# Performance work log

Hardware: AMD Instinct MI355X
Metric: run time of the kernel (lower is better)

The kernel has to match this reference:

```python
import jax, jax.numpy as jnp
import numpy as np

# Model hyperparams (match init_kwargs)
B, T, CIN, COUT = 4, 12, 4, 4
P = 16; HIMG = WIMG = 256; HP = WP = 16
D = 384; L = 4; DFF = 4 * D; MAXG = 0.3
CPLX = jnp.complex64

# NOTE: RiemannianCliffordConv2d / TemporalPropagator / FluxTracker / basis /
# encoder / decoder sources were not provided; they are reconstructed here as
# faithful-structure surrogates: plain conv2d for the Clifford conv, complex
# linear eigen-basis encode/decode, exp-decay scan operators, complex FFN,
# patch-embed conv encoder and per-patch linear decoder. sde_mode='ode' so the
# stochastic branch is skipped, matching the explicit guard in the source.

def _ln(x, g, b):
    m = x.mean(-1, keepdims=True)
    v = jnp.var(x, axis=-1, keepdims=True)
    return (x - m) * jax.lax.rsqrt(v + 1e-5) * g + b

def _conv(x, w, b, stride, pad):
    y = jax.lax.conv_general_dilated(x, w, (stride, stride), pad,
                                     dimension_numbers=('NCHW', 'OIHW', 'NCHW'))
    return y + b[None, :, None, None]

def _pscan(A, X):
    # first-order linear recurrence h_t = A_t*h_{t-1} + X_t via associative scan over axis=1
    def comb(l, r):
        al, xl = l; ar, xr = r
        return al * ar, xl * ar + xr
    return jax.lax.associative_scan(comb, (A, X), axis=1)[1]

def _cgelu(z):
    return jax.nn.gelu(z.real) + 1j * jax.nn.gelu(z.imag)

def _model(x, dt, enc_w, enc_b, ns_g, ns_b, cw, cb, nt_g, nt_b,
           E_re, E_im, Ei_re, Ei_im, lam_flux, Ws_re, Ws_im, Wg, nu, omega,
           w1_re, w1_im, w2_re, w2_im, dec_w, dec_b):
    Bx, Tx = x.shape[0], x.shape[1]
    # ---- encoder: patch-embed conv -> complex latent (B,T,D,HP,WP)
    xf = x.reshape(Bx * Tx, CIN, HIMG, WIMG)
    e = _conv(xf, enc_w, enc_b, P, 'VALID')              # (BT, 2D, HP, WP)
    zr, zi = jnp.split(e, 2, axis=1)
    z = (zr + 1j * zi).astype(CPLX).reshape(Bx, Tx, D, HP, WP)
    for i in range(L):
        E = E_re[i] + 1j * E_im[i]
        Ei = Ei_re[i] + 1j * Ei_im[i]
        Ws = Ws_re[i] + 1j * Ws_im[i]
        W1 = w1_re[i] + 1j * w1_im[i]
        W2 = w2_re[i] + 1j * w2_im[i]
        # ---- _apply_spatial (residual Clifford conv on stacked re/im)
        xflat = z.reshape(Bx * Tx, D, HP, WP)
        xr2 = jnp.concatenate([xflat.real, xflat.imag], axis=1)   # (BT,2D,H,W)
        xn = jnp.transpose(xr2, (0, 2, 3, 1))
        xn = _ln(xn, ns_g[i], ns_b[i])
        xn = jnp.transpose(xn, (0, 3, 1, 2))
        xs = _conv(xn, cw[i], cb[i], 1, 'SAME')
        sre, sim = jnp.split(xs, 2, axis=1)
        xflat = xflat + (sre + 1j * sim)
        z = xflat.reshape(Bx, Tx, D, HP, WP)
        # ---- eigen-basis encode
        xp = jnp.transpose(z, (0, 1, 3, 4, 2))                    # (B,T,H,W,D)
        x_eig = jnp.einsum('bthwd,de->bthwe', xp, E)
        x_mean = x_eig.mean(axis=(2, 3))                          # (B,T,D)
        # ---- flux tracker scan (states start at zero => flux_prev term vanishes)
        a = jnp.exp(-jax.nn.softplus(lam_flux[i])[None, None] * dt[..., None])
        A_flux = a.astype(CPLX)
        X_flux = x_mean * dt[..., None]
        flux = _pscan(A_flux, X_flux)                             # (B,T,D) complex
        source = jnp.einsum('btd,de->bte', flux, Ws)
        gate = jax.nn.sigmoid(flux.real * Wg[i][None, None])      # (B,T,D) real
        g = gate[:, :, None, None, :]
        forcing = x_eig * g + source[:, :, None, None, :] * (1.0 - g)
        # ---- transition operators and temporal pscan
        lam = jnp.clip(-jax.nn.softplus(nu[i]), -5.0, MAXG) + 1j * omega[i]  # (D,)
        op_decay = jnp.exp(lam[None, None] * dt[..., None])       # (B,T,D) complex
        op_forcing = (op_decay - 1.0) / lam
        u_t = forcing * op_forcing[:, :, None, None, :]           # (B,T,H,W,D)
        # h_prev is zero-initialized per _init_states => its t0 contribution is zero
        A_full = jnp.broadcast_to(op_decay[:, :, None, None, :], u_t.shape)
        u_out = _pscan(A_full, u_t)                               # (B,T,H,W,D)
        # ---- decode + temporal FFN residual
        decoded = jnp.einsum('bthwd,de->bthwe', u_out, Ei)
        dec5 = jnp.transpose(decoded, (0, 1, 4, 2, 3))            # (B,T,D,H,W)
        df = dec5.reshape(Bx * Tx, D, HP, WP)
        dr = jnp.concatenate([df.real, df.imag], axis=1)
        dn = _ln(jnp.transpose(dr, (0, 2, 3, 1)), nt_g[i], nt_b[i])
        dn = jnp.transpose(dn, (0, 3, 1, 2))
        nre, nim = jnp.split(dn, 2, axis=1)
        xcl = jnp.transpose(nre + 1j * nim, (0, 2, 3, 1))          # (BT,H,W,D)
        delta = jnp.einsum('bhwf,fd->bhwd', _cgelu(jnp.einsum('bhwd,df->bhwf', xcl, W1)), W2)
        delta = jnp.transpose(delta, (0, 3, 1, 2))
        x_out = (df + delta).reshape(Bx, Tx, D, HP, WP)
        z = z + x_out
    # ---- ensemble decoder (mean member): per-patch linear head + depth-to-space
    feats = jnp.concatenate([z.real, z.imag], axis=2)             # (B,T,2D,H,W)
    fl = jnp.transpose(feats, (0, 1, 3, 4, 2))                    # (B,T,H,W,2D)
    y = jnp.einsum('bthwc,oc->bthwo', fl, dec_w) + dec_b
    y = y.reshape(Bx, Tx, HP, WP, COUT, P, P)
    y = jnp.transpose(y, (0, 1, 4, 2, 5, 3, 6)).reshape(Bx, Tx, COUT, HP * P, WP * P)
    return y


def setup_inputs() -> dict:
    key = jax.random.key(0)
    ks = jax.random.split(key, 32)
    s = 0.02
    d = {}
    d['x'] = jax.random.normal(ks[0], (B, T, CIN, HIMG, WIMG), dtype=jnp.float32)
    d['dt'] = jax.random.uniform(ks[1], (B, T), minval=0.5, maxval=1.5, dtype=jnp.float32)
    d['enc_w'] = jax.random.normal(ks[2], (2 * D, CIN, P, P), dtype=jnp.float32) * s
    d['enc_b'] = jnp.zeros((2 * D,), jnp.float32)
    d['ns_g'] = jnp.ones((L, 2 * D), jnp.float32)
    d['ns_b'] = jnp.zeros((L, 2 * D), jnp.float32)
    d['cw'] = jax.random.normal(ks[3], (L, 2 * D, 2 * D, 3, 3), dtype=jnp.float32) * s
    d['cb'] = jnp.zeros((L, 2 * D), jnp.float32)
    d['nt_g'] = jnp.ones((L, 2 * D), jnp.float32)
    d['nt_b'] = jnp.zeros((L, 2 * D), jnp.float32)
    d['E_re'] = jax.random.normal(ks[4], (L, D, D), dtype=jnp.float32) * s
    d['E_im'] = jax.random.normal(ks[5], (L, D, D), dtype=jnp.float32) * s
    d['Ei_re'] = jax.random.normal(ks[6], (L, D, D), dtype=jnp.float32) * s
    d['Ei_im'] = jax.random.normal(ks[7], (L, D, D), dtype=jnp.float32) * s
    d['lam_flux'] = jax.random.normal(ks[8], (L, D), dtype=jnp.float32)
    d['Ws_re'] = jax.random.normal(ks[9], (L, D, D), dtype=jnp.float32) * s
    d['Ws_im'] = jax.random.normal(ks[10], (L, D, D), dtype=jnp.float32) * s
    d['Wg'] = jax.random.normal(ks[11], (L, D), dtype=jnp.float32)
    d['nu'] = jax.random.normal(ks[12], (L, D), dtype=jnp.float32)
    d['omega'] = jax.random.normal(ks[13], (L, D), dtype=jnp.float32) * 0.5
    d['w1_re'] = jax.random.normal(ks[14], (L, D, DFF), dtype=jnp.float32) * s
    d['w1_im'] = jax.random.normal(ks[15], (L, D, DFF), dtype=jnp.float32) * s
    d['w2_re'] = jax.random.normal(ks[16], (L, DFF, D), dtype=jnp.float32) * s
    d['w2_im'] = jax.random.normal(ks[17], (L, DFF, D), dtype=jnp.float32) * s
    d['dec_w'] = jax.random.normal(ks[18], (COUT * P * P, 2 * D), dtype=jnp.float32) * s
    d['dec_b'] = jnp.zeros((COUT * P * P,), jnp.float32)
    return d


def reference(x, dt, enc_w, enc_b, ns_g, ns_b, cw, cb, nt_g, nt_b,
              E_re, E_im, Ei_re, Ei_im, lam_flux, Ws_re, Ws_im, Wg, nu, omega,
              w1_re, w1_im, w2_re, w2_im, dec_w, dec_b):
    return _model(x, dt, enc_w, enc_b, ns_g, ns_b, cw, cb, nt_g, nt_b,
                  E_re, E_im, Ei_re, Ei_im, lam_flux, Ws_re, Ws_im, Wg, nu, omega,
                  w1_re, w1_im, w2_re, w2_im, dec_w, dec_b)
```

## Files before the change

kernel.cpp:

```cpp
#include <hip/hip_runtime.h>
#include <cstddef>
#include <cstdint>

typedef unsigned short u16;
typedef short bf16x8 __attribute__((ext_vector_type(8)));
typedef float f32x4 __attribute__((ext_vector_type(4)));

__device__ __forceinline__ float gelu_tanh(float x) {
  float x3 = x * x * x;
  float t = tanhf(0.7978845608028654f * (x + 0.044715f * x3));
  return 0.5f * x * (1.0f + t);
}
__device__ __forceinline__ float softplus_f(float x) {
  return (x > 20.0f) ? x : log1pf(expf(x));
}
__device__ __forceinline__ u16 f2bf(float f) {
  uint32_t u = __float_as_uint(f);
  uint32_t r = (u + 0x7fffu + ((u >> 16) & 1u)) >> 16;
  return (u16)r;
}

__device__ __forceinline__ void gload16(const u16* g, u16* l) {
  __builtin_amdgcn_global_load_lds(
      (const __attribute__((address_space(1))) void*)g,
      (__attribute__((address_space(3))) void*)l, 16, 0, 0);
}

template <int TN, int MODE>
__global__ __launch_bounds__(256) void gemm_kernel(
    const u16* __restrict__ A, const u16* __restrict__ Bt, int K, int ldc,
    float* __restrict__ Cf, u16* __restrict__ Cb,
    const float* __restrict__ bias, const float* __restrict__ Df) {
  __shared__ u16 As[2][128 * 32];
  __shared__ u16 Bs[2][TN * 32];
  constexpr int NI = (TN == 64) ? 2 : 4;
  const int m0 = blockIdx.x * 128, n0 = blockIdx.y * TN;
  const int tid = threadIdx.x;
  const int lane = tid & 63, w = tid >> 6;
  const int lane15 = lane & 15, quad = lane >> 4;
  const int r0 = lane >> 2, e0 = (lane & 3) * 8;
  const int wy = (TN == 64) ? w : (w >> 1);
  const int wx = (TN == 64) ? 0 : (w & 1);

  const u16* ag0 = A + (size_t)(m0 + w * 32 + r0) * K + e0;
  const u16* ag1 = ag0 + (size_t)16 * K;
  const u16* bg0 = (TN == 64) ? Bt + (size_t)(n0 + w * 16 + r0) * K + e0
                              : Bt + (size_t)(n0 + w * 32 + r0) * K + e0;
  const u16* bg1 = bg0 + (size_t)16 * K;

  f32x4 acc[NI][4] = {};
  const int abase = (wy * (16 * NI) + lane15) * 32 + quad * 8;
  const int bbase = (wx * 64 + lane15) * 32 + quad * 8;

  for (int k0 = 0; k0 < K; k0 += 64) {
#pragma unroll
    for (int p = 0; p < 2; ++p) {
      const int kk = k0 + 32 * p;
      gload16(ag0 + kk, &As[p][w * 1024]);
      gload16(ag1 + kk, &As[p][w * 1024 + 512]);
      if (TN == 64) {
        gload16(bg0 + kk, &Bs[p][w * 512]);
      } else {
        gload16(bg0 + kk, &Bs[p][w * 1024]);
        gload16(bg1 + kk, &Bs[p][w * 1024 + 512]);
      }
    }
    __syncthreads();
#pragma unroll
    for (int p = 0; p < 2; ++p) {
      bf16x8 af[NI], bf[4];
#pragma unroll
      for (int i = 0; i < NI; ++i) af[i] = *(const bf16x8*)&As[p][abase + i * 16 * 32];
#pragma unroll
      for (int j = 0; j < 4; ++j) bf[j] = *(const bf16x8*)&Bs[p][bbase + j * 16 * 32];
#pragma unroll
      for (int i = 0; i < NI; ++i)
#pragma unroll
        for (int j = 0; j < 4; ++j)
          acc[i][j] = __builtin_amdgcn_mfma_f32_16x16x32_bf16(af[i], bf[j], acc[i][j], 0, 0, 0);
    }
    __syncthreads();
  }

  const int mw = m0 + wy * (16 * NI), nw = n0 + wx * 64;
#pragma unroll
  for (int i = 0; i < NI; ++i) {
#pragma unroll
    for (int j = 0; j < 4; ++j) {
      const int col = nw + j * 16 + lane15;
#pragma unroll
      for (int r = 0; r < 4; ++r) {
        const int row = mw + i * 16 + quad * 4 + r;
        const float v = acc[i][j][r];
        const size_t idx = (size_t)row * ldc + col;
        if (MODE == 0) {
          Cf[idx] = v;
        } else if (MODE == 1) {
          Cb[idx] = f2bf(gelu_tanh(v));
        } else if (MODE == 2) {
          Cf[idx] += v;
        } else if (MODE == 3) {
          const int frame = row >> 8, pix = row & 255;
          const int hp = pix >> 4, wp = pix & 15;
          const int co = col >> 8, p1 = (col >> 4) & 15, p2 = col & 15;
          Cf[(((size_t)frame * 4 + co) * 256 + hp * 16 + p1) * 256 + wp * 16 + p2] = v + bias[col];
        } else if (MODE == 4) {
          Cf[idx] += v + Df[idx];
        } else if (MODE == 5) {
          const float nz = Cf[idx] + v;
          Cf[idx] = nz;
          Cb[idx] = f2bf(nz);
        }
      }
    }
  }
}

__global__ __launch_bounds__(256) void conv_mfma_kernel(
    const u16* __restrict__ xnp, const u16* __restrict__ Btc,
    const float* __restrict__ cbias,
    float* __restrict__ z, u16* __restrict__ zb) {
  __shared__ u16 As[2][128 * 32];
  __shared__ u16 Bs[2][128 * 32];
  const int m0 = blockIdx.x * 128, n0 = blockIdx.y * 128;
  const int tid = threadIdx.x;
  const int lane = tid & 63, w = tid >> 6;
  const int lane15 = lane & 15, quad = lane >> 4;
  const int r0 = lane >> 2, e0 = (lane & 3) * 8;

  const int rowA0 = m0 + w * 32 + r0, rowA1 = rowA0 + 16;
  const long long cen0 = ((long long)(rowA0 >> 8) * 324 + ((((rowA0 & 255) >> 4) + 1) * 18) + (rowA0 & 15) + 1) * 768 + e0;
  const long long cen1 = ((long long)(rowA1 >> 8) * 324 + ((((rowA1 & 255) >> 4) + 1) * 18) + (rowA1 & 15) + 1) * 768 + e0;
  const u16* bg0 = Btc + (size_t)(n0 + w * 32 + r0) * 6912 + e0;
  const u16* bg1 = bg0 + (size_t)16 * 6912;

  f32x4 acc[4][4] = {};
  const int wy = w >> 1, wx = w & 1;
  const int abase = (wy * 64 + lane15) * 32 + quad * 8;
  const int bbase = (wx * 64 + lane15) * 32 + quad * 8;

  for (int tap = 0; tap < 9; ++tap) {
    const int doff = ((tap / 3 - 1) * 18 + (tap % 3 - 1)) * 768;
    const u16* a0 = xnp + cen0 + doff;
    const u16* a1 = xnp + cen1 + doff;
    const u16* b0 = bg0 + tap * 768;
    const u16* b1 = bg1 + tap * 768;
    for (int kc = 0; kc < 768; kc += 64) {
#pragma unroll
      for (int p = 0; p < 2; ++p) {
        const int kk = kc + 32 * p;
        gload16(a0 + kk, &As[p][w * 1024]);
        gload16(a1 + kk, &As[p][w * 1024 + 512]);
        gload16(b0 + kk, &Bs[p][w * 1024]);
        gload16(b1 + kk, &Bs[p][w * 1024 + 512]);
      }
      __syncthreads();
#pragma unroll
      for (int p = 0; p < 2; ++p) {
        bf16x8 af[4], bf[4];
#pragma unroll
        for (int i = 0; i < 4; ++i) af[i] = *(const bf16x8*)&As[p][abase + i * 16 * 32];
#pragma unroll
        for (int j = 0; j < 4; ++j) bf[j] = *(const bf16x8*)&Bs[p][bbase + j * 16 * 32];
#pragma unroll
        for (int i = 0; i < 4; ++i)
#pragma unroll
          for (int j = 0; j < 4; ++j)
            acc[i][j] = __builtin_amdgcn_mfma_f32_16x16x32_bf16(af[i], bf[j], acc[i][j], 0, 0, 0);
      }
      __syncthreads();
    }
  }

  const int mw = m0 + wy * 64, nw = n0 + wx * 64;
#pragma unroll
  for (int i = 0; i < 4; ++i) {
#pragma unroll
    for (int j = 0; j < 4; ++j) {
      const int col = nw + j * 16 + lane15;
      const float bv = cbias[col];
#pragma unroll
      for (int r = 0; r < 4; ++r) {
        const int row = mw + i * 16 + quad * 4 + r;
        const size_t idx = (size_t)row * 768 + col;
        const float nz = z[idx] + acc[i][j][r] + bv;
        z[idx] = nz;
        zb[idx] = f2bf(nz);
      }
    }
  }
}

__global__ __launch_bounds__(256) void encoder_mfma_kernel(
    const float* __restrict__ x, const float* __restrict__ ew,
    const float* __restrict__ eb, float* __restrict__ z) {
  __shared__ u16 As[128 * 32];
  __shared__ u16 Bs[128 * 32];
  const int m0 = blockIdx.x * 128, n0 = blockIdx.y * 128;
  const int tid = threadIdx.x;
  const int lane = tid & 63, w = tid >> 6;
  const int lane15 = lane & 15, quad = lane >> 4;
  const int srow = tid >> 1, half = tid & 1;
  const int arow = m0 + srow;
  const int frame = arow >> 8, pix = arow & 255, hh = pix >> 4, ww = pix & 15;

  f32x4 acc[4][4] = {};
  const int wy = w >> 1, wx = w & 1;
  const int ar_base = (wy * 64 + lane15) * 32 + quad * 8;
  const int br_base = (wx * 64 + lane15) * 32 + quad * 8;

  for (int k0 = 0; k0 < 1024; k0 += 32) {
    const int gk = k0 + half * 16;
    const int c = gk >> 8, ph = (gk >> 4) & 15;
    const float* ax = x + (((size_t)(frame * 4 + c) * 256 + hh * 16 + ph) * 256 + ww * 16);
    const float* bx = ew + (size_t)(n0 + srow) * 1024 + gk;
    u16 ta[16], tb[16];
#pragma unroll
    for (int j = 0; j < 4; ++j) {
      const float4 va = *(const float4*)(ax + j * 4);
      const float4 vb = *(const float4*)(bx + j * 4);
      ta[j * 4 + 0] = f2bf(va.x); ta[j * 4 + 1] = f2bf(va.y);
      ta[j * 4 + 2] = f2bf(va.z); ta[j * 4 + 3] = f2bf(va.w);
      tb[j * 4 + 0] = f2bf(vb.x); tb[j * 4 + 1] = f2bf(vb.y);
      tb[j * 4 + 2] = f2bf(vb.z); tb[j * 4 + 3] = f2bf(vb.w);
    }
    __syncthreads();
    *(uint4*)&As[srow * 32 + half * 16] = *(uint4*)ta;
    *(uint4*)&As[srow * 32 + half * 16 + 8] = *(uint4*)(ta + 8);
    *(uint4*)&Bs[srow * 32 + half * 16] = *(uint4*)tb;
    *(uint4*)&Bs[srow * 32 + half * 16 + 8] = *(uint4*)(tb + 8);
    __syncthreads();
    bf16x8 af[4], bfv[4];
#pragma unroll
    for (int i = 0; i < 4; ++i) af[i] = *(const bf16x8*)&As[ar_base + i * 16 * 32];
#pragma unroll
    for (int j = 0; j < 4; ++j) bfv[j] = *(const bf16x8*)&Bs[br_base + j * 16 * 32];
#pragma unroll
    for (int i = 0; i < 4; ++i)
#pragma unroll
      for (int j = 0; j < 4; ++j)
        acc[i][j] = __builtin_amdgcn_mfma_f32_16x16x32_bf16(af[i], bfv[j], acc[i][j], 0, 0, 0);
  }

  const int mw = m0 + wy * 64, nw = n0 + wx * 64;
#pragma unroll
  for (int i = 0; i < 4; ++i)
#pragma unroll
    for (int j = 0; j < 4; ++j) {
      const int col = nw + j * 16 + lane15;
      const float bv = eb[col];
#pragma unroll
      for (int r = 0; r < 4; ++r) {
        const int row = mw + i * 16 + quad * 4 + r;
        z[(size_t)row * 768 + col] = acc[i][j][r] + bv;
      }
    }
}

__global__ __launch_bounds__(256) void expand_kernel(
    const float* __restrict__ Wre, const float* __restrict__ Wim,
    int ldw, int Kc, int Nc, u16* __restrict__ Wt) {
  __shared__ float tile[32][33];
  const int k0 = blockIdx.x * 32, n0 = blockIdx.y * 32;
  const bool khi = k0 >= Kc, nhi = n0 >= Nc;
  const float* src = (khi != nhi) ? Wim : Wre;
  const float sgn = (!nhi && khi) ? -1.0f : 1.0f;
  const int sk = k0 - (khi ? Kc : 0), sn = n0 - (nhi ? Nc : 0);
  const int c = threadIdx.x & 31, r8 = threadIdx.x >> 5;
  for (int r = r8; r < 32; r += 8)
    tile[r][c] = src[(size_t)(sk + r) * ldw + sn + c];
  __syncthreads();
  const int twoK = 2 * Kc;
  for (int r = r8; r < 32; r += 8)
    Wt[(size_t)(n0 + r) * twoK + k0 + c] = f2bf(sgn * tile[c][r]);
}

__global__ __launch_bounds__(256) void reorder_cw_kernel(
    const float* __restrict__ cwl, u16* __restrict__ Btc) {
  __shared__ float buf[6912];
  const int o = blockIdx.x;
  const float* src = cwl + (size_t)o * 6912;
  for (int i = threadIdx.x; i < 6912; i += 256) buf[i] = src[i];
  __syncthreads();
  u16* dst = Btc + (size_t)o * 6912;
  for (int i = threadIdx.x; i < 6912; i += 256) {
    const int tap = i / 768, cc = i - tap * 768;
    dst[i] = f2bf(buf[cc * 9 + tap]);
  }
}

__global__ __launch_bounds__(256) void cast_bf16_kernel(
    const float* __restrict__ in, u16* __restrict__ out, int n) {
  const int g = blockIdx.x * 256 + threadIdx.x;
  if (g < n) out[g] = f2bf(in[g]);
}

template <bool HALO>
__global__ __launch_bounds__(192) void ln_kernel(
    const float* __restrict__ in, const float* __restrict__ g,
    const float* __restrict__ b, u16* __restrict__ out) {
  const int row = blockIdx.x, tid = threadIdx.x;
  const float4 v = *(const float4*)(in + (size_t)row * 768 + tid * 4);
  float s = v.x + v.y + v.z + v.w;
  float q = v.x * v.x + v.y * v.y + v.z * v.z + v.w * v.w;
#pragma unroll
  for (int off = 32; off > 0; off >>= 1) {
    s += __shfl_down(s, off);
    q += __shfl_down(q, off);
  }
  __shared__ float rs[3], rq[3];
  if ((tid & 63) == 0) { rs[tid >> 6] = s; rq[tid >> 6] = q; }
  __syncthreads();
  const float S = rs[0] + rs[1] + rs[2], Q = rq[0] + rq[1] + rq[2];
  const float mean = S * (1.0f / 768.0f);
  const float inv = rsqrtf(Q * (1.0f / 768.0f) - mean * mean + 1e-5f);
  const float4 gv = *(const float4*)(g + tid * 4);
  const float4 bv = *(const float4*)(b + tid * 4);
  u16 p[4];
  p[0] = f2bf((v.x - mean) * inv * gv.x + bv.x);
  p[1] = f2bf((v.y - mean) * inv * gv.y + bv.y);
  p[2] = f2bf((v.z - mean) * inv * gv.z + bv.z);
  p[3] = f2bf((v.w - mean) * inv * gv.w + bv.w);
  size_t base;
  if (HALO) {
    const int f = row >> 8, pp = row & 255, h = pp >> 4, ww = pp & 15;
    base = ((size_t)f * 324 + (h + 1) * 18 + ww + 1) * 768;
  } else {
    base = (size_t)row * 768;
  }
  *(uint2*)(out + base + tid * 4) = *(uint2*)p;
}

__global__ __launch_bounds__(768) void mean_kernel(
    const float* __restrict__ eig, float* __restrict__ mr, float* __restrict__ mi) {
  const int f = blockIdx.x, c = threadIdx.x;
  const float* p = eig + (size_t)f * 256 * 768 + c;
  float s0 = 0.f, s1 = 0.f, s2 = 0.f, s3 = 0.f;
  for (int px = 0; px < 256; px += 4) {
    s0 += p[(size_t)px * 768];
    s1 += p[(size_t)(px + 1) * 768];
    s2 += p[(size_t)(px + 2) * 768];
    s3 += p[(size_t)(px + 3) * 768];
  }
  const float tot = (s0 + s1 + s2 + s3) * (1.0f / 256.0f);
  if (c < 384) mr[f * 384 + c] = tot;
  else         mi[f * 384 + c - 384] = tot;
}

__global__ __launch_bounds__(384) void flux_kernel(
    const float* __restrict__ dt, const float* __restrict__ lamf,
    const float* __restrict__ nu, const float* __restrict__ omega,
    const float* __restrict__ mr, const float* __restrict__ mi,
    float* __restrict__ fluxr, float* __restrict__ fluxi,
    float* __restrict__ opdr, float* __restrict__ opdi,
    float* __restrict__ opfr, float* __restrict__ opfi) {
  const int b = blockIdx.x;
  const int d = threadIdx.x;
  const float sp = softplus_f(lamf[d]);
  float lre = -softplus_f(nu[d]);
  lre = fmaxf(lre, -5.0f);
  const float lim = omega[d];
  const float den = lre * lre + lim * lim;
  float fr = 0.f, fi = 0.f;
  for (int t = 0; t < 12; ++t) {
    const float dtv = dt[b * 12 + t];
    const int idx = (b * 12 + t) * 384 + d;
    const float A = expf(-sp * dtv);
    fr = A * fr + mr[idx] * dtv;
    fi = A * fi + mi[idx] * dtv;
    fluxr[idx] = fr; fluxi[idx] = fi;
    const float ed = expf(lre * dtv);
    const float odr = ed * cosf(lim * dtv);
    const float odi = ed * sinf(lim * dtv);
    opdr[idx] = odr; opdi[idx] = odi;
    const float nr_ = odr - 1.0f, ni_ = odi;
    opfr[idx] = (nr_ * lre + ni_ * lim) / den;
    opfi[idx] = (ni_ * lre - nr_ * lim) / den;
  }
}

#define SBM 64
#define SBN 64
#define SBK 32
__global__ __launch_bounds__(256) void cgemm_src_kernel(
    const float* __restrict__ Ar, const float* __restrict__ Ai, int lda,
    const float* __restrict__ Wr, const float* __restrict__ Wi, int ldw,
    const float* __restrict__ Wg,
    float* __restrict__ G, float* __restrict__ SGr, float* __restrict__ SGi,
    int ldc, int M, int K) {
  __shared__ float Asr[SBK][SBM], Asi[SBK][SBM];
  __shared__ float Wsr[SBK][SBN], Wsi[SBK][SBN];
  const int m0 = blockIdx.x * SBM;
  const int n0 = blockIdx.y * SBN;
  const int tid = threadIdx.x;
  const int tn = tid & 15, tm = tid >> 4;
  float accr[4][4] = {}, acci[4][4] = {};
  for (int k0 = 0; k0 < K; k0 += SBK) {
    for (int s = tid; s < 512; s += 256) {
      {
        int r = s >> 3, kk = (s & 7) << 2;
        int row = m0 + r;
        float4 vr = {0.f, 0.f, 0.f, 0.f}, vi = {0.f, 0.f, 0.f, 0.f};
        if (row < M) {
          vr = *(const float4*)(Ar + (size_t)row * lda + k0 + kk);
          vi = *(const float4*)(Ai + (size_t)row * lda + k0 + kk);
        }
        Asr[kk + 0][r] = vr.x; Asr[kk + 1][r] = vr.y; Asr[kk + 2][r] = vr.z; Asr[kk + 3][r] = vr.w;
        Asi[kk + 0][r] = vi.x; Asi[kk + 1][r] = vi.y; Asi[kk + 2][r] = vi.z; Asi[kk + 3][r] = vi.w;
      }
      {
        int wr_ = s >> 4, wc = (s & 15) << 2;
        *(float4*)&Wsr[wr_][wc] = *(const float4*)(Wr + (size_t)(k0 + wr_) * ldw + n0 + wc);
        *(float4*)&Wsi[wr_][wc] = *(const float4*)(Wi + (size_t)(k0 + wr_) * ldw + n0 + wc);
      }
    }
    __syncthreads();
#pragma unroll
    for (int kk = 0; kk < SBK; ++kk) {
      float4 ar4 = *(const float4*)&Asr[kk][tm << 2];
      float4 ai4 = *(const float4*)&Asi[kk][tm << 2];
      float4 wr4 = *(const float4*)&Wsr[kk][tn << 2];
      float4 wi4 = *(const float4*)&Wsi[kk][tn << 2];
      float ar[4] = {ar4.x, ar4.y, ar4.z, ar4.w};
      float ai[4] = {ai4.x, ai4.y, ai4.z, ai4.w};
      float wr[4] = {wr4.x, wr4.y, wr4.z, wr4.w};
      float wi[4] = {wi4.x, wi4.y, wi4.z, wi4.w};
#pragma unroll
      for (int i = 0; i < 4; ++i)
#pragma unroll
        for (int j = 0; j < 4; ++j) {
          accr[i][j] = fmaf(ar[i], wr[j], accr[i][j]);
          accr[i][j] = fmaf(-ai[i], wi[j], accr[i][j]);
          acci[i][j] = fmaf(ar[i], wi[j], acci[i][j]);
          acci[i][j] = fmaf(ai[i], wr[j], acci[i][j]);
        }
    }
    __syncthreads();
  }
#pragma unroll
  for (int i = 0; i < 4; ++i) {
    int row = m0 + (tm << 2) + i;
    if (row >= M) continue;
#pragma unroll
    for (int j = 0; j < 4; ++j) {
      int col = n0 + (tn << 2) + j;
      size_t idx = (size_t)row * ldc + col;
      const float gate = 1.0f / (1.0f + expf(-Ar[idx] * Wg[col]));
      G[idx] = gate;
      SGr[idx] = accr[i][j] * (1.0f - gate);
      SGi[idx] = acci[i][j] * (1.0f - gate);
    }
  }
}

__global__ __launch_bounds__(256) void pscan_fused_kernel(
    const float* __restrict__ eig,
    const float* __restrict__ Gv,
    const float* __restrict__ SGr, const float* __restrict__ SGi,
    const float* __restrict__ opfr, const float* __restrict__ opfi,
    const float* __restrict__ opdr, const float* __restrict__ opdi,
    u16* __restrict__ ub) {
  const int g = blockIdx.x * 256 + threadIdx.x;
  if (g >= 4 * 256 * 384) return;
  const int d = g % 384;
  const int pix = (g / 384) & 255;
  const int b = g / (384 * 256);
  float ur = 0.f, ui = 0.f;
  for (int t = 0; t < 12; ++t) {
    const int frame = b * 12 + t;
    const size_t idx = ((size_t)frame * 256 + pix) * 768 + d;
    const int fidx = frame * 384 + d;
    const float G = Gv[fidx];
    const float fr = eig[idx] * G + SGr[fidx];
    const float fi = eig[idx + 384] * G + SGi[fidx];
    const float pr = opfr[fidx], pi = opfi[fidx];
    const float utr = fr * pr - fi * pi;
    const float uti = fr * pi + fi * pr;
    const float ar = opdr[fidx], ai = opdi[fidx];
    const float nr = ar * ur - ai * ui + utr;
    const float ni = ar * ui + ai * ur + uti;
    ub[idx] = f2bf(nr); ub[idx + 384] = f2bf(ni);
    ur = nr; ui = ni;
  }
}

extern "C" void kernel_launch(void* const* d_in, const int* in_sizes, int n_in,
                              void* d_out, int out_size, void* d_ws, size_t ws_size,
                              hipStream_t stream) {
  const float* x        = (const float*)d_in[0];
  const float* dt       = (const float*)d_in[1];
  const float* enc_w    = (const float*)d_in[2];
  const float* enc_b    = (const float*)d_in[3];
  const float* ns_g     = (const float*)d_in[4];
  const float* ns_b     = (const float*)d_in[5];
  const float* cw       = (const float*)d_in[6];
  const float* cb       = (const float*)d_in[7];
  const float* nt_g     = (const float*)d_in[8];
  const float* nt_b     = (const float*)d_in[9];
  const float* E_re     = (const float*)d_in[10];
  const float* E_im     = (const float*)d_in[11];
  const float* Ei_re    = (const float*)d_in[12];
  const float* Ei_im    = (const float*)d_in[13];
  const float* lam_flux = (const float*)d_in[14];
  const float* Ws_re    = (const float*)d_in[15];
  const float* Ws_im    = (const float*)d_in[16];
  const float* Wg       = (const float*)d_in[17];
  const float* nu       = (const float*)d_in[18];
  const float* omega    = (const float*)d_in[19];
  const float* w1_re    = (const float*)d_in[20];
  const float* w1_im    = (const float*)d_in[21];
  const float* w2_re    = (const float*)d_in[22];
  const float* w2_im    = (const float*)d_in[23];
  const float* dec_w    = (const float*)d_in[24];
  const float* dec_b    = (const float*)d_in[25];
  float* out = (float*)d_out;

  const size_t NPF = 12288ull * 768;
  const size_t XNP = 48ull * 324 * 768;
  const size_t SM = 48ull * 384;

  float* z   = (float*)d_ws;
  float* eig = z + NPF;
  float* df  = eig + NPF;
  u16* xnp   = (u16*)(df + NPF);
  u16* Btc   = xnp + XNP;
  u16* Et    = Btc + 5308416;
  u16* Eit   = Et + 589824;
  u16* W1t   = Eit + 589824;
  u16* W2t   = W1t + 2359296;
  u16* dwt   = W2t + 2359296;
  float* sm  = (float*)(dwt + 786432);
  float* mr    = sm;            float* mi    = mr + SM;
  float* fluxr = mi + SM;       float* fluxi = fluxr + SM;
  float* opdr  = fluxi + SM;    float* opdi  = opdr + SM;
  float* opfr  = opdi + SM;     float* opfi  = opfr + SM;
  float* Gv    = opfi + SM;     float* SGr   = Gv + SM;
  float* SGi   = SGr + SM;

  const size_t need = ((char*)(SGi + SM)) - ((char*)d_ws);
  if (ws_size < need) return;

  u16* zb  = (u16*)df;
  u16* h1b = (u16*)eig;

  cast_bf16_kernel<<<(786432 + 255) / 256, 256, 0, stream>>>(dec_w, dwt, 786432);
  encoder_mfma_kernel<<<dim3(96, 6), 256, 0, stream>>>(x, enc_w, enc_b, z);

  for (int l = 0; l < 4; ++l) {
    const size_t DD = 384ull * 384, DF = 384ull * 1536;
    hipMemsetAsync(xnp, 0, XNP * sizeof(u16), stream);
    reorder_cw_kernel<<<768, 256, 0, stream>>>(cw + (size_t)l * 768 * 768 * 9, Btc);
    expand_kernel<<<dim3(24, 24), 256, 0, stream>>>(E_re + l * DD, E_im + l * DD, 384, 384, 384, Et);
    expand_kernel<<<dim3(24, 24), 256, 0, stream>>>(Ei_re + l * DD, Ei_im + l * DD, 384, 384, 384, Eit);
    for (int ch = 0; ch < 2; ++ch) {
      expand_kernel<<<dim3(24, 48), 256, 0, stream>>>(
          w1_re + l * DF + ch * 768, w1_im + l * DF + ch * 768, 1536, 384, 768, W1t + (size_t)ch * 1179648);
      expand_kernel<<<dim3(48, 24), 256, 0, stream>>>(
          w2_re + l * DF + (size_t)ch * 768 * 384, w2_im + l * DF + (size_t)ch * 768 * 384, 384, 768, 384,
          W2t + (size_t)ch * 1179648);
    }

    ln_kernel<true><<<12288, 192, 0, stream>>>(z, ns_g + l * 768, ns_b + l * 768, xnp);
    conv_mfma_kernel<<<dim3(96, 6), 256, 0, stream>>>(xnp, Btc, cb + l * 768, z, zb);
    gemm_kernel<64, 0><<<dim3(96, 12), 256, 0, stream>>>(zb, Et, 768, 768, eig, nullptr, nullptr, nullptr);
    mean_kernel<<<48, 768, 0, stream>>>(eig, mr, mi);
    flux_kernel<<<4, 384, 0, stream>>>(dt, lam_flux + l * 384, nu + l * 384, omega + l * 384,
                                       mr, mi, fluxr, fluxi, opdr, opdi, opfr, opfi);
    cgemm_src_kernel<<<dim3(1, 6), 256, 0, stream>>>(
        fluxr, fluxi, 384, Ws_re + l * DD, Ws_im + l * DD, 384,
        Wg + l * 384, Gv, SGr, SGi, 384, 48, 384);
    pscan_fused_kernel<<<1536, 256, 0, stream>>>(eig, Gv, SGr, SGi, opfr, opfi, opdr, opdi, xnp);
    gemm_kernel<64, 0><<<dim3(96, 12), 256, 0, stream>>>(xnp, Eit, 768, 768, df, nullptr, nullptr, nullptr);
    ln_kernel<false><<<12288, 192, 0, stream>>>(df, nt_g + l * 768, nt_b + l * 768, xnp);
    for (int ch = 0; ch < 2; ++ch) {
      gemm_kernel<128, 1><<<dim3(96, 12), 256, 0, stream>>>(
          xnp, W1t + (size_t)ch * 1179648, 768, 1536, nullptr, h1b, nullptr, nullptr);
      if (ch == 0) {
        gemm_kernel<64, 4><<<dim3(96, 12), 256, 0, stream>>>(
            h1b, W2t, 1536, 768, z, nullptr, nullptr, df);
      } else if (l < 3) {
        gemm_kernel<64, 2><<<dim3(96, 12), 256, 0, stream>>>(
            h1b, W2t + 1179648, 1536, 768, z, nullptr, nullptr, nullptr);
      } else {
        gemm_kernel<64, 5><<<dim3(96, 12), 256, 0, stream>>>(
            h1b, W2t + 1179648, 1536, 768, z, zb, nullptr, nullptr);
      }
    }
  }

  gemm_kernel<64, 3><<<dim3(96, 16), 256, 0, stream>>>(zb, dwt, 768, 0, out, nullptr, dec_b, nullptr);
}
```

Before: 2.828 ms.

## Split conv taps across grid z with atomic accumulation and swizzle GEMM block order

The 3x3 conv GEMM grid is split three ways along the tap (K) dimension, and the partial sums are accumulated into z with float atomics. This triples the number of blocks from 576 to 1728 so the 256 CUs are better occupied. Because atomics cannot produce the bf16 copy, a separate vectorized cast kernel now writes zb after the conv. The GEMM and conv kernels also remap block IDs with an 8-way swizzle to change scheduling order and cache locality. The cost is atomic traffic, nondeterministic summation order, and one extra pass over z.

Result: slower. 3.310 ms (+17.0%).

```diff
diff --git a/kernel.cpp b/kernel.cpp
--- a/kernel.cpp
+++ b/kernel.cpp
@@ -34,7 +34,10 @@
   __shared__ u16 As[2][128 * 32];
   __shared__ u16 Bs[2][TN * 32];
   constexpr int NI = (TN == 64) ? 2 : 4;
-  const int m0 = blockIdx.x * 128, n0 = blockIdx.y * TN;
+  const int total8 = (gridDim.x * gridDim.y) >> 3;
+  const int lid = blockIdx.x + gridDim.x * blockIdx.y;
+  const int gsw = (lid & 7) * total8 + (lid >> 3);
+  const int m0 = (gsw % gridDim.x) * 128, n0 = (gsw / gridDim.x) * TN;
   const int tid = threadIdx.x;
   const int lane = tid & 63, w = tid >> 6;
   const int lane15 = lane & 15, quad = lane >> 4;
@@ -118,11 +121,14 @@
 
 __global__ __launch_bounds__(256) void conv_mfma_kernel(
     const u16* __restrict__ xnp, const u16* __restrict__ Btc,
-    const float* __restrict__ cbias,
-    float* __restrict__ z, u16* __restrict__ zb) {
+    const float* __restrict__ cbias, float* __restrict__ z) {
   __shared__ u16 As[2][128 * 32];
   __shared__ u16 Bs[2][128 * 32];
-  const int m0 = blockIdx.x * 128, n0 = blockIdx.y * 128;
+  const int lid = blockIdx.x + 96 * (blockIdx.y + 6 * blockIdx.z);
+  const int gsw = (lid & 7) * 216 + (lid >> 3);
+  const int zi = gsw / 576;
+  const int rem = gsw - zi * 576;
+  const int m0 = (rem % 96) * 128, n0 = (rem / 96) * 128;
   const int tid = threadIdx.x;
   const int lane = tid & 63, w = tid >> 6;
   const int lane15 = lane & 15, quad = lane >> 4;
@@ -139,7 +145,7 @@
   const int abase = (wy * 64 + lane15) * 32 + quad * 8;
   const int bbase = (wx * 64 + lane15) * 32 + quad * 8;
 
-  for (int tap = 0; tap < 9; ++tap) {
+  for (int tap = 3 * zi; tap < 3 * zi + 3; ++tap) {
     const int doff = ((tap / 3 - 1) * 18 + (tap % 3 - 1)) * 768;
     const u16* a0 = xnp + cen0 + doff;
     const u16* a1 = xnp + cen1 + doff;
@@ -178,14 +184,11 @@
 #pragma unroll
     for (int j = 0; j < 4; ++j) {
       const int col = nw + j * 16 + lane15;
-      const float bv = cbias[col];
+      const float bv = (zi == 0) ? cbias[col] : 0.0f;
 #pragma unroll
       for (int r = 0; r < 4; ++r) {
         const int row = mw + i * 16 + quad * 4 + r;
-        const size_t idx = (size_t)row * 768 + col;
-        const float nz = z[idx] + acc[i][j][r] + bv;
-        z[idx] = nz;
-        zb[idx] = f2bf(nz);
+        atomicAdd(&z[(size_t)row * 768 + col], acc[i][j][r] + bv);
       }
     }
   }
@@ -293,6 +296,16 @@
     const float* __restrict__ in, u16* __restrict__ out, int n) {
   const int g = blockIdx.x * 256 + threadIdx.x;
   if (g < n) out[g] = f2bf(in[g]);
+}
+
+__global__ __launch_bounds__(256) void cast_bf16x4_kernel(
+    const float* __restrict__ in, u16* __restrict__ out, int n4) {
+  const int g = blockIdx.x * 256 + threadIdx.x;
+  if (g < n4) {
+    const float4 v = *(const float4*)(in + (size_t)g * 4);
+    u16 p[4] = {f2bf(v.x), f2bf(v.y), f2bf(v.z), f2bf(v.w)};
+    *(uint2*)(out + (size_t)g * 4) = *(uint2*)p;
+  }
 }
 
 template <bool HALO>
@@ -561,7 +574,8 @@
     }
 
     ln_kernel<true><<<12288, 192, 0, stream>>>(z, ns_g + l * 768, ns_b + l * 768, xnp);
-    conv_mfma_kernel<<<dim3(96, 6), 256, 0, stream>>>(xnp, Btc, cb + l * 768, z, zb);
+    conv_mfma_kernel<<<dim3(96, 6, 3), 256, 0, stream>>>(xnp, Btc, cb + l * 768, z);
+    cast_bf16x4_kernel<<<(int)((NPF / 4 + 255) / 256), 256, 0, stream>>>(z, zb, (int)(NPF / 4));
     gemm_kernel<64, 0><<<dim3(96, 12), 256, 0, stream>>>(zb, Et, 768, 768, eig, nullptr, nullptr, nullptr);
     mean_kernel<<<48, 768, 0, stream>>>(eig, mr, mi);
     flux_kernel<<<4, 384, 0, stream>>>(dt, lam_flux + l * 384, nu + l * 384, omega + l * 384,
```
